# Optimization experiments

Hardware: AMD Instinct MI355X
Metric: run time of the kernel (lower is better)

Reference implementation:

```python
import jax, jax.numpy as jnp
import numpy as np

N_LAYER = 2
N_HEAD = 12
D = 768
B = 4
L = 1024
LN_EPS = 1e-6
NEG = jnp.float32(-1e9)


def setup_inputs() -> dict:
    key = jax.random.key(0)
    ks = jax.random.split(key, 12)
    s = 0.02
    wshp = (N_LAYER, 4, D, D)
    return {
        "h_a": jax.random.normal(ks[0], (B, L, D), jnp.float32),
        "h_b": jax.random.normal(ks[1], (B, L, D), jnp.float32),
        "adj_a": jax.random.randint(ks[2], (B, L, L), 0, 2, jnp.int32),
        "adj_b": jax.random.randint(ks[3], (B, L, L), 0, 2, jnp.int32),
        "adj_ab": jax.random.randint(ks[4], (B, L, L), 0, 2, jnp.int32),
        "adj_ba": jax.random.randint(ks[5], (B, L, L), 0, 2, jnp.int32),
        "Wq": jax.random.normal(ks[6], wshp, jnp.float32) * s,
        "Wk": jax.random.normal(ks[7], wshp, jnp.float32) * s,
        "Wv": jax.random.normal(ks[8], wshp, jnp.float32) * s,
        "Wf": jax.random.normal(ks[9], wshp, jnp.float32) * s,
        "ln_g": jnp.ones((N_LAYER, 4, D), jnp.float32),
        "ln_b": jnp.zeros((N_LAYER, 4, D), jnp.float32),
    }


def _mha(xq, xk, xv, mask, Wq, Wk, Wv, Wf, g, b):
    # xq: [B, Lq, D]; mask: [B, Lq, Lk] (0 = masked out)
    Bq, Lq, d = xq.shape
    dk = d // N_HEAD
    q = (xq @ Wq).reshape(Bq, Lq, N_HEAD, dk).transpose(0, 2, 1, 3)
    k = (xk @ Wk).reshape(Bq, -1, N_HEAD, dk).transpose(0, 2, 1, 3)
    v = (xv @ Wv).reshape(Bq, -1, N_HEAD, dk).transpose(0, 2, 1, 3)
    attn = jnp.einsum('bhqd,bhkd->bhqk', q, k) / jnp.sqrt(jnp.float32(dk))
    attn = jnp.where(mask[:, None, :, :] == 0, NEG, attn)
    attn = jax.nn.softmax(attn, axis=-1)
    o = jnp.einsum('bhqk,bhkd->bhqd', attn, v)
    o = o.transpose(0, 2, 1, 3).reshape(Bq, Lq, d)
    o = o @ Wf + xq  # residual (dropout is identity in eval)
    mu = jnp.mean(o, axis=-1, keepdims=True)
    var = jnp.var(o, axis=-1, keepdims=True)
    return (o - mu) * jax.lax.rsqrt(var + LN_EPS) * g + b


def reference(h_a, h_b, adj_a, adj_b, adj_ab, adj_ba, Wq, Wk, Wv, Wf, ln_g, ln_b):
    input_a, input_b = h_a, h_b
    for i in range(N_LAYER):
        a2a = _mha(h_a, h_a, h_a, adj_a, Wq[i, 0], Wk[i, 0], Wv[i, 0], Wf[i, 0], ln_g[i, 0], ln_b[i, 0])
        b2b = _mha(h_b, h_b, h_b, adj_b, Wq[i, 1], Wk[i, 1], Wv[i, 1], Wf[i, 1], ln_g[i, 1], ln_b[i, 1])
        a2b = _mha(h_b, h_a, h_a, adj_ab, Wq[i, 2], Wk[i, 2], Wv[i, 2], Wf[i, 2], ln_g[i, 2], ln_b[i, 2])
        b2a = _mha(h_a, h_b, h_b, adj_ba, Wq[i, 3], Wk[i, 3], Wv[i, 3], Wf[i, 3], ln_g[i, 3], ln_b[i, 3])
        h_a = jax.nn.relu(a2a + b2a)
        h_b = jax.nn.relu(b2b + a2b)
    return (input_a + h_a, input_b + h_b)
```

## Files before the change

### kernel.cpp

```cpp
#include <hip/hip_runtime.h>
#include <stdint.h>

#define NLAYER 2
#define NHEAD 12
#define D 768
#define BB 4
#define LL 1024
#define M (BB*LL)
#define DK 64
#define CSC 0.1803368801111204f

typedef unsigned short u16;
typedef unsigned int u32;
typedef unsigned long long u64;
typedef __attribute__((ext_vector_type(8))) __bf16 bf16x8;
typedef __attribute__((ext_vector_type(4))) float f32x4;

__device__ __forceinline__ u16 f2b(float f) {
  u32 u = __float_as_uint(f);
  u += 0x7fffu + ((u >> 16) & 1u);
  return (u16)(u >> 16);
}
__device__ __forceinline__ float b2f(u16 h) {
  return __uint_as_float(((u32)h) << 16);
}
__device__ __forceinline__ f32x4 mfma16(bf16x8 a, bf16x8 b, f32x4 c) {
  return __builtin_amdgcn_mfma_f32_16x16x32_bf16(a, b, c, 0, 0, 0);
}
__device__ __forceinline__ void gl_lds16(const u16* g, u16* l) {
  __builtin_amdgcn_global_load_lds((const __attribute__((address_space(1))) void*)(g),
                                   (__attribute__((address_space(3))) void*)(l), 16, 0, 0);
}

__global__ void cast_f32_bf16(const float* __restrict__ src, u16* __restrict__ dst, int n) {
  int i = (blockIdx.x * 256 + threadIdx.x) * 4;
  if (i + 3 < n) {
    float4 v = *(const float4*)(src + i);
    dst[i+0] = f2b(v.x); dst[i+1] = f2b(v.y); dst[i+2] = f2b(v.z); dst[i+3] = f2b(v.w);
  }
}

__global__ void wtrans(const float* __restrict__ Wq, const float* __restrict__ Wk,
                       const float* __restrict__ Wv, const float* __restrict__ Wf,
                       u16* __restrict__ wtr) {
  int z = blockIdx.z;
  int layer = z >> 4, mat = (z >> 2) & 3, s = z & 3;
  const float* src = (mat==0?Wq:mat==1?Wk:mat==2?Wv:Wf) + (size_t)(layer*4 + s)*D*D;
  u16* dst = wtr + (size_t)z*D*D;
  __shared__ float tile[32][33];
  int x0 = blockIdx.x*32, y0 = blockIdx.y*32;
  int tx = threadIdx.x & 31, ty = threadIdx.x >> 5;
  #pragma unroll
  for (int i=0;i<4;++i) tile[ty + i*8][tx] = src[(size_t)(y0 + ty + i*8)*D + x0 + tx];
  __syncthreads();
  #pragma unroll
  for (int i=0;i<4;++i) dst[(size_t)(x0 + ty + i*8)*D + y0 + tx] = f2b(tile[tx][ty + i*8]);
}

__global__ __launch_bounds__(256) void pack_adj(const int* __restrict__ a0, const int* __restrict__ a1,
                                                const int* __restrict__ a2, const int* __restrict__ a3,
                                                u64* __restrict__ mb) {
  const int s = blockIdx.y;
  const int* __restrict__ src = s==0?a0:s==1?a1:s==2?a2:a3;
  u64* dst = mb + (size_t)s * (BB*LL*LL/64);
  const int lane = threadIdx.x & 63;
  const int w0 = blockIdx.x*4 + (threadIdx.x>>6);
  const int wstep = gridDim.x*4;
  for (int w = w0; w < BB*LL*LL/64; w += wstep) {
    int v = src[(size_t)w*64 + lane];
    u64 m = __ballot(v != 0);
    if (lane == 0) dst[w] = m;
  }
}

__device__ __forceinline__ void gemm128(const u16* __restrict__ A, const u16* __restrict__ W,
                                        u16* __restrict__ C, int cmode,
                                        int m0, int n0) {
  __shared__ __align__(16) u16 As[2][128*32];
  __shared__ __align__(16) u16 Bs[2][128*32];
  const int t = threadIdx.x;
  const int wave = t >> 6, lane = t & 63, lg = lane >> 4, lr = lane & 15;
  const int wr = wave >> 2, wc = wave & 3;
  f32x4 acc[4][2] = {};
  const int srow = wave*16 + (lane >> 2);
  const int scol = (lane & 3) << 3;
  const u16* ga0 = A + (size_t)(m0 + srow)*D + scol;
  const u16* gb0 = W + (size_t)(n0 + srow)*D + scol;
  const int l0 = (wave*16)*32;

  for (int kk = 0; kk < D; kk += 64) {
    __syncthreads();
    #pragma unroll
    for (int hh=0; hh<2; ++hh) {
      const int ko = kk + hh*32;
      gl_lds16(ga0 + ko, &As[hh][l0]);
      gl_lds16(gb0 + ko, &Bs[hh][l0]);
    }
    __syncthreads();
    #pragma unroll
    for (int hh=0; hh<2; ++hh) {
      bf16x8 af[4], bfr[2];
      #pragma unroll
      for (int mi=0;mi<4;++mi) af[mi] = *(const bf16x8*)(&As[hh][(wr*64 + mi*16 + lr)*32 + lg*8]);
      #pragma unroll
      for (int ni=0;ni<2;++ni) bfr[ni] = *(const bf16x8*)(&Bs[hh][(wc*32 + ni*16 + lr)*32 + lg*8]);
      #pragma unroll
      for (int mi=0;mi<4;++mi)
        #pragma unroll
        for (int ni=0;ni<2;++ni)
          acc[mi][ni] = mfma16(af[mi], bfr[ni], acc[mi][ni]);
    }
  }

  if (cmode != 1) {
    const float scl = (cmode == 2) ? CSC : 1.0f;
    #pragma unroll
    for (int mi=0;mi<4;++mi)
      #pragma unroll
      for (int ni=0;ni<2;++ni) {
        int col = n0 + wc*32 + ni*16 + lr;
        #pragma unroll
        for (int r=0;r<4;++r) {
          int row = m0 + wr*64 + mi*16 + lg*4 + r;
          C[(size_t)row*D + col] = f2b(acc[mi][ni][r] * scl);
        }
      }
  } else {
    #pragma unroll
    for (int mi=0;mi<4;++mi)
      #pragma unroll
      for (int ni=0;ni<2;++ni) {
        int col = n0 + wc*32 + ni*16 + lr;
        int h = col >> 6, d = col & 63;
        #pragma unroll
        for (int r=0;r<4;++r) {
          int row = m0 + wr*64 + mi*16 + lg*4 + r;
          int p = ((r >> 1) << 5) | (lg << 3) | (mi << 1) | (r & 1);
          int lperm = (row & ~63) | p;
          int b = row >> 10, l = lperm & 1023;
          C[(((size_t)((b*NHEAD + h)<<6) + d) << 10) + l] = f2b(acc[mi][ni][r]);
        }
      }
  }
}

__global__ __launch_bounds__(512) void qkv_gemm(const u16* __restrict__ hA, const u16* __restrict__ hB,
                        const u16* __restrict__ wtr,
                        u16* __restrict__ Qb, u16* __restrict__ Kb, u16* __restrict__ Vtb, int layer) {
  int bid = blockIdx.x + 32*(blockIdx.y + 6*blockIdx.z);
  int logical = (bid & 7)*288 + (bid >> 3);
  int z = logical / 192, rem = logical % 192;
  int x = rem / 6, y = rem % 6;
  int s = z / 3, which = z % 3;
  const u16* X;
  if (which == 0) X = (s==0||s==3) ? hA : hB;
  else            X = (s==0||s==2) ? hA : hB;
  const u16* W = wtr + (size_t)((layer*4 + which)*4 + s)*D*D;
  u16* Cb = (which==0 ? Qb : which==1 ? Kb : Vtb) + (size_t)s*M*D;
  gemm128(X, W, Cb, which == 2 ? 1 : (which == 0 ? 2 : 0), x*128, y*128);
}

__global__ __launch_bounds__(512) void oproj_gemm(const u16* __restrict__ Ob, const u16* __restrict__ wtr,
                          u16* __restrict__ OPb, int layer) {
  int bid = blockIdx.x + 32*(blockIdx.y + 6*blockIdx.z);
  int logical = (bid & 7)*96 + (bid >> 3);
  int s = logical / 192, rem = logical % 192;
  int x = rem / 6, y = rem % 6;
  const u16* W = wtr + (size_t)((layer*4 + 3)*4 + s)*D*D;
  gemm128(Ob + (size_t)s*M*D, W, OPb + (size_t)s*M*D, 0, x*128, y*128);
}

__global__ __launch_bounds__(512) void attn_kernel(const u16* __restrict__ Qb, const u16* __restrict__ Kb,
                           const u16* __restrict__ Vtb,
                           const u64* __restrict__ mbits,
                           u16* __restrict__ Ob) {
  int bid = blockIdx.x + 8*(blockIdx.y + 48*blockIdx.z);
  int logical = (bid & 7)*192 + (bid >> 3);
  const int qt = logical & 7;
  const int bhs = logical >> 3;
  const int s = bhs / 48;
  const int bh = bhs % 48;
  const int b = bh / NHEAD, h = bh % NHEAD;

  const int t = threadIdx.x, wave = t >> 6, lane = t & 63, lg = lane >> 4, lr = lane & 15;
  const u16* Q = Qb + (size_t)s*M*D;
  const u16* K = Kb + (size_t)s*M*D;
  u16* O = Ob + (size_t)s*M*D;
  const u64* mbs = mbits + (size_t)s*(BB*LL*LL/64) + (size_t)b*(LL*LL/64);

  __shared__ __align__(16) u16 Ks[64][72];
  __shared__ __align__(16) u16 Vts[64][72];

  const int q0 = qt*128 + wave*16;
  bf16x8 qf0 = *(const bf16x8*)(Q + (size_t)(b*LL + q0 + lr)*D + h*DK + lg*8);
  bf16x8 qf1 = *(const bf16x8*)(Q + (size_t)(b*LL + q0 + lr)*D + h*DK + 32 + lg*8);

  f32x4 of[4] = {};
  float lrow = 0.f;

  const int kr = t >> 3, kc = (t & 7) << 3;
  const u16* Kp  = K + (size_t)(b*LL + kr)*D + h*DK + kc;
  const u16* Vtp = Vtb + (size_t)s*M*D + ((size_t)(bh*64 + kr) << 10) + kc;

  uint4 ka = *(const uint4*)(Kp);
  uint4 va = *(const uint4*)(Vtp);
  const int mstride = LL/64;
  u64 mw = mbs[(size_t)(q0 + lr)*mstride];
  u64 mwn;

  for (int kt = 0; kt < LL; kt += 64) {
    __syncthreads();
    *(uint4*)(&Ks[kr][kc])  = ka;
    *(uint4*)(&Vts[kr][kc]) = va;
    if (kt + 64 < LL) {
      ka = *(const uint4*)(Kp + (size_t)(kt+64)*D);
      va = *(const uint4*)(Vtp + kt + 64);
      mwn = mbs[(size_t)(q0 + lr)*mstride + (kt >> 6) + 1];
    }
    __syncthreads();

    f32x4 sfr[4];
    __builtin_amdgcn_s_setprio(1);
    #pragma unroll
    for (int c=0;c<4;++c) {
      bf16x8 kf0 = *(const bf16x8*)(&Ks[c*16+lr][lg*8]);
      bf16x8 kf1 = *(const bf16x8*)(&Ks[c*16+lr][32 + lg*8]);
      f32x4 z = {0.f,0.f,0.f,0.f};
      z = mfma16(kf0, qf0, z);
      z = mfma16(kf1, qf1, z);
      sfr[c] = z;
    }
    __builtin_amdgcn_s_setprio(0);

    u32 wlo = (u32)(mw >> (lg*4));
    u32 whi = (u32)(mw >> (lg*4 + 32));
    float pw[4][4];
    #pragma unroll
    for (int c=0;c<4;++c) {
      u32 wsel = (c < 2) ? wlo : whi;
      int sh = (c & 1) << 4;
      #pragma unroll
      for (int r=0;r<4;++r) {
        float e = __builtin_amdgcn_exp2f(sfr[c][r]);
        e = ((wsel >> (sh + r)) & 1u) ? e : 0.f;
        pw[c][r] = e;
        lrow += e;
      }
    }
    mw = mwn;

    union { u32 u[4]; bf16x8 v; } a0, a1;
    #pragma unroll
    for (int c=0;c<4;++c) {
      a0.u[c] = (__float_as_uint(pw[c][0]) >> 16) | (__float_as_uint(pw[c][1]) & 0xffff0000u);
      a1.u[c] = (__float_as_uint(pw[c][2]) >> 16) | (__float_as_uint(pw[c][3]) & 0xffff0000u);
    }

    __builtin_amdgcn_s_setprio(1);
    #pragma unroll
    for (int ni=0;ni<4;++ni) {
      bf16x8 vf0 = *(const bf16x8*)(&Vts[ni*16+lr][lg*8]);
      bf16x8 vf1 = *(const bf16x8*)(&Vts[ni*16+lr][32 + lg*8]);
      of[ni] = mfma16(a0.v, vf0, of[ni]);
      of[ni] = mfma16(a1.v, vf1, of[ni]);
    }
    __builtin_amdgcn_s_setprio(0);
  }

  lrow += __shfl_xor(lrow, 16, 64);
  lrow += __shfl_xor(lrow, 32, 64);

  #pragma unroll
  for (int r=0;r<4;++r) {
    float l = __shfl(lrow, lg*4 + r, 64);
    float inv = 1.0f / fmaxf(l, 1e-35f);
    int row = b*LL + q0 + lg*4 + r;
    #pragma unroll
    for (int ni=0;ni<4;++ni)
      O[(size_t)row*D + h*DK + ni*16 + lr] = f2b(of[ni][r] * inv);
  }
}

__global__ __launch_bounds__(256) void epilogue(const u16* __restrict__ OPb,
                        u16* __restrict__ hA, u16* __restrict__ hB,
                        const float* __restrict__ lng, const float* __restrict__ lnb,
                        const float* __restrict__ inA, const float* __restrict__ inB,
                        float* __restrict__ outA, float* __restrict__ outB,
                        int layer, int last) {
  const int row = blockIdx.x;
  const int t = threadIdx.x;
  __shared__ float red[4][8];
  float av[3], bv[3];
  #pragma unroll
  for (int j=0;j<3;++j) {
    int c = t + j*256;
    av[j] = b2f(hA[(size_t)row*D + c]);
    bv[j] = b2f(hB[(size_t)row*D + c]);
  }
  float o[4][3]; float sum[4] = {0,0,0,0}, sq[4] = {0,0,0,0};
  #pragma unroll
  for (int s=0;s<4;++s) {
    #pragma unroll
    for (int j=0;j<3;++j) {
      int c = t + j*256;
      float v = b2f(OPb[((size_t)s*M + row)*D + c]) + ((s==0||s==3) ? av[j] : bv[j]);
      o[s][j]=v; sum[s]+=v; sq[s]+=v*v;
    }
  }
  #pragma unroll
  for (int off=32; off>0; off>>=1)
    #pragma unroll
    for (int s=0;s<4;++s) { sum[s] += __shfl_down(sum[s], off, 64); sq[s] += __shfl_down(sq[s], off, 64); }
  int wv = t>>6, ln = t&63;
  if (ln==0) {
    #pragma unroll
    for (int s=0;s<4;++s) { red[wv][s] = sum[s]; red[wv][4+s] = sq[s]; }
  }
  __syncthreads();
  float lnv[4][3];
  #pragma unroll
  for (int s=0;s<4;++s) {
    float sm = red[0][s]+red[1][s]+red[2][s]+red[3][s];
    float sk = red[0][4+s]+red[1][4+s]+red[2][4+s]+red[3][4+s];
    float mu = sm * (1.0f/D);
    float var = sk * (1.0f/D) - mu*mu;
    float rstd = rsqrtf(var + 1e-6f);
    #pragma unroll
    for (int j=0;j<3;++j) {
      int c = t + j*256;
      lnv[s][j] = (o[s][j]-mu)*rstd * lng[(layer*4+s)*D + c] + lnb[(layer*4+s)*D + c];
    }
  }
  #pragma unroll
  for (int j=0;j<3;++j) {
    int c = t + j*256;
    float ha = fmaxf(lnv[0][j]+lnv[3][j], 0.f);
    float hb = fmaxf(lnv[1][j]+lnv[2][j], 0.f);
    hA[(size_t)row*D + c] = f2b(ha);
    hB[(size_t)row*D + c] = f2b(hb);
    if (last) {
      outA[(size_t)row*D + c] = inA[(size_t)row*D + c] + ha;
      outB[(size_t)row*D + c] = inB[(size_t)row*D + c] + hb;
    }
  }
}

extern "C" void kernel_launch(void* const* d_in, const int* in_sizes, int n_in,
                              void* d_out, int out_size, void* d_ws, size_t ws_size,
                              hipStream_t stream) {
  const float* h_a = (const float*)d_in[0];
  const float* h_b = (const float*)d_in[1];
  const int* adjA  = (const int*)d_in[2];
  const int* adjB  = (const int*)d_in[3];
  const int* adjAB = (const int*)d_in[4];
  const int* adjBA = (const int*)d_in[5];
  const float* Wq  = (const float*)d_in[6];
  const float* Wk  = (const float*)d_in[7];
  const float* Wv  = (const float*)d_in[8];
  const float* Wf  = (const float*)d_in[9];
  const float* lng = (const float*)d_in[10];
  const float* lnb = (const float*)d_in[11];
  float* outA = (float*)d_out;
  float* outB = outA + (size_t)M*D;

  char* ws = (char*)d_ws;
  size_t off = 0;
  auto alloc = [&](size_t bytes) { void* p = ws + off; off += (bytes + 255) & ~(size_t)255; return p; };
  u16* wtr = (u16*)alloc((size_t)32*D*D*2);
  u16* hAb = (u16*)alloc((size_t)M*D*2);
  u16* hBb = (u16*)alloc((size_t)M*D*2);
  u16* Qb  = (u16*)alloc((size_t)4*M*D*2);
  u16* Kb  = (u16*)alloc((size_t)4*M*D*2);
  u16* Vtb = (u16*)alloc((size_t)4*M*D*2);
  u16* Ob  = (u16*)alloc((size_t)4*M*D*2);
  u64* mbits = (u64*)alloc((size_t)4*BB*LL*LL/64*8);
  u16* OPb = Qb;

  int n = M*D;
  cast_f32_bf16<<<dim3(n/4/256), 256, 0, stream>>>(h_a, hAb, n);
  cast_f32_bf16<<<dim3(n/4/256), 256, 0, stream>>>(h_b, hBb, n);
  wtrans<<<dim3(24,24,32), 256, 0, stream>>>(Wq, Wk, Wv, Wf, wtr);
  pack_adj<<<dim3(2048,4), 256, 0, stream>>>(adjA, adjB, adjAB, adjBA, mbits);

  for (int layer = 0; layer < NLAYER; ++layer) {
    qkv_gemm<<<dim3(32,6,12), 512, 0, stream>>>(hAb, hBb, wtr, Qb, Kb, Vtb, layer);
    attn_kernel<<<dim3(8,48,4), 512, 0, stream>>>(Qb, Kb, Vtb, mbits, Ob);
    oproj_gemm<<<dim3(32,6,4), 512, 0, stream>>>(Ob, wtr, OPb, layer);
    epilogue<<<dim3(M), 256, 0, stream>>>(OPb, hAb, hBb, lng, lnb, h_a, h_b, outA, outB,
                                          layer, layer == NLAYER-1 ? 1 : 0);
  }
}
```

Measured before the change: 429.5 us.

## Switch attention to 32x32x16 MFMA with 32-query waves and larger q tiles

Result: slower. 458.0 us (+6.6%).

```diff
diff --git a/kernel.cpp b/kernel.cpp
--- a/kernel.cpp
+++ b/kernel.cpp
@@ -15,6 +15,7 @@
 typedef unsigned long long u64;
 typedef __attribute__((ext_vector_type(8))) __bf16 bf16x8;
 typedef __attribute__((ext_vector_type(4))) float f32x4;
+typedef __attribute__((ext_vector_type(16))) float f32x16;
 
 __device__ __forceinline__ u16 f2b(float f) {
   u32 u = __float_as_uint(f);
@@ -26,6 +27,9 @@
 }
 __device__ __forceinline__ f32x4 mfma16(bf16x8 a, bf16x8 b, f32x4 c) {
   return __builtin_amdgcn_mfma_f32_16x16x32_bf16(a, b, c, 0, 0, 0);
+}
+__device__ __forceinline__ f32x16 mfma32(bf16x8 a, bf16x8 b, f32x16 c) {
+  return __builtin_amdgcn_mfma_f32_32x32x16_bf16(a, b, c, 0, 0, 0);
 }
 __device__ __forceinline__ void gl_lds16(const u16* g, u16* l) {
   __builtin_amdgcn_global_load_lds((const __attribute__((address_space(1))) void*)(g),
@@ -135,9 +139,7 @@
         #pragma unroll
         for (int r=0;r<4;++r) {
           int row = m0 + wr*64 + mi*16 + lg*4 + r;
-          int p = ((r >> 1) << 5) | (lg << 3) | (mi << 1) | (r & 1);
-          int lperm = (row & ~63) | p;
-          int b = row >> 10, l = lperm & 1023;
+          int b = row >> 10, l = row & 1023;
           C[(((size_t)((b*NHEAD + h)<<6) + d) << 10) + l] = f2b(acc[mi][ni][r]);
         }
       }
@@ -174,15 +176,16 @@
                            const u16* __restrict__ Vtb,
                            const u64* __restrict__ mbits,
                            u16* __restrict__ Ob) {
-  int bid = blockIdx.x + 8*(blockIdx.y + 48*blockIdx.z);
-  int logical = (bid & 7)*192 + (bid >> 3);
-  const int qt = logical & 7;
-  const int bhs = logical >> 3;
+  int bid = blockIdx.x + 4*(blockIdx.y + 48*blockIdx.z);
+  int logical = (bid & 7)*96 + (bid >> 3);
+  const int qt = logical & 3;
+  const int bhs = logical >> 2;
   const int s = bhs / 48;
   const int bh = bhs % 48;
   const int b = bh / NHEAD, h = bh % NHEAD;
 
-  const int t = threadIdx.x, wave = t >> 6, lane = t & 63, lg = lane >> 4, lr = lane & 15;
+  const int t = threadIdx.x, wave = t >> 6, lane = t & 63;
+  const int ql = lane & 31, hi = lane >> 5;
   const u16* Q = Qb + (size_t)s*M*D;
   const u16* K = Kb + (size_t)s*M*D;
   u16* O = Ob + (size_t)s*M*D;
@@ -191,11 +194,14 @@
   __shared__ __align__(16) u16 Ks[64][72];
   __shared__ __align__(16) u16 Vts[64][72];
 
-  const int q0 = qt*128 + wave*16;
-  bf16x8 qf0 = *(const bf16x8*)(Q + (size_t)(b*LL + q0 + lr)*D + h*DK + lg*8);
-  bf16x8 qf1 = *(const bf16x8*)(Q + (size_t)(b*LL + q0 + lr)*D + h*DK + 32 + lg*8);
-
-  f32x4 of[4] = {};
+  const int q0 = qt*256 + wave*32;
+  const int q = q0 + ql;
+  bf16x8 qf[4];
+  #pragma unroll
+  for (int kk=0;kk<4;++kk)
+    qf[kk] = *(const bf16x8*)(Q + (size_t)(b*LL + q)*D + h*DK + kk*16 + hi*8);
+
+  f32x16 of[2] = {};
   float lrow = 0.f;
 
   const int kr = t >> 3, kc = (t & 7) << 3;
@@ -205,7 +211,7 @@
   uint4 ka = *(const uint4*)(Kp);
   uint4 va = *(const uint4*)(Vtp);
   const int mstride = LL/64;
-  u64 mw = mbs[(size_t)(q0 + lr)*mstride];
+  u64 mw = mbs[(size_t)q*mstride];
   u64 mwn;
 
   for (int kt = 0; kt < LL; kt += 64) {
@@ -215,70 +221,82 @@
     if (kt + 64 < LL) {
       ka = *(const uint4*)(Kp + (size_t)(kt+64)*D);
       va = *(const uint4*)(Vtp + kt + 64);
-      mwn = mbs[(size_t)(q0 + lr)*mstride + (kt >> 6) + 1];
+      mwn = mbs[(size_t)q*mstride + (kt >> 6) + 1];
     }
     __syncthreads();
 
-    f32x4 sfr[4];
-    __builtin_amdgcn_s_setprio(1);
-    #pragma unroll
-    for (int c=0;c<4;++c) {
-      bf16x8 kf0 = *(const bf16x8*)(&Ks[c*16+lr][lg*8]);
-      bf16x8 kf1 = *(const bf16x8*)(&Ks[c*16+lr][32 + lg*8]);
-      f32x4 z = {0.f,0.f,0.f,0.f};
-      z = mfma16(kf0, qf0, z);
-      z = mfma16(kf1, qf1, z);
-      sfr[c] = z;
-    }
-    __builtin_amdgcn_s_setprio(0);
-
-    u32 wlo = (u32)(mw >> (lg*4));
-    u32 whi = (u32)(mw >> (lg*4 + 32));
-    float pw[4][4];
-    #pragma unroll
-    for (int c=0;c<4;++c) {
-      u32 wsel = (c < 2) ? wlo : whi;
-      int sh = (c & 1) << 4;
-      #pragma unroll
-      for (int r=0;r<4;++r) {
-        float e = __builtin_amdgcn_exp2f(sfr[c][r]);
-        e = ((wsel >> (sh + r)) & 1u) ? e : 0.f;
-        pw[c][r] = e;
-        lrow += e;
-      }
+    #pragma unroll
+    for (int kb=0; kb<2; ++kb) {
+      f32x16 S = {};
+      __builtin_amdgcn_s_setprio(1);
+      #pragma unroll
+      for (int kk=0;kk<4;++kk) {
+        bf16x8 kf = *(const bf16x8*)(&Ks[kb*32 + ql][kk*16 + hi*8]);
+        S = mfma32(kf, qf[kk], S);
+      }
+      __builtin_amdgcn_s_setprio(0);
+
+      u32 wm = (u32)(mw >> (kb*32 + 4*hi));
+      float pv[16];
+      #pragma unroll
+      for (int p=0;p<4;++p)
+        #pragma unroll
+        for (int r=0;r<4;++r) {
+          float e = __builtin_amdgcn_exp2f(S[4*p+r]);
+          e = ((wm >> (r + 8*p)) & 1u) ? e : 0.f;
+          pv[4*p+r] = e;
+          lrow += e;
+        }
+
+      u32 pk[4][2];
+      #pragma unroll
+      for (int p=0;p<4;++p) {
+        pk[p][0] = ((u32)f2b(pv[4*p+0])) | (((u32)f2b(pv[4*p+1]))<<16);
+        pk[p][1] = ((u32)f2b(pv[4*p+2])) | (((u32)f2b(pv[4*p+3]))<<16);
+      }
+      u32 recv[2][2];
+      #pragma unroll
+      for (int s2=0;s2<2;++s2)
+        #pragma unroll
+        for (int w2=0;w2<2;++w2) {
+          u32 snd = hi ? pk[2*s2][w2] : pk[2*s2+1][w2];
+          recv[s2][w2] = (u32)__shfl_xor((int)snd, 32, 64);
+        }
+      union { u32 u[4]; bf16x8 v; } pf0, pf1;
+      if (hi == 0) {
+        pf0.u[0]=pk[0][0]; pf0.u[1]=pk[0][1]; pf0.u[2]=recv[0][0]; pf0.u[3]=recv[0][1];
+        pf1.u[0]=pk[2][0]; pf1.u[1]=pk[2][1]; pf1.u[2]=recv[1][0]; pf1.u[3]=recv[1][1];
+      } else {
+        pf0.u[0]=recv[0][0]; pf0.u[1]=recv[0][1]; pf0.u[2]=pk[1][0]; pf0.u[3]=pk[1][1];
+        pf1.u[0]=recv[1][0]; pf1.u[1]=recv[1][1]; pf1.u[2]=pk[3][0]; pf1.u[3]=pk[3][1];
+      }
+
+      __builtin_amdgcn_s_setprio(1);
+      #pragma unroll
+      for (int db=0; db<2; ++db) {
+        bf16x8 vf0 = *(const bf16x8*)(&Vts[db*32 + ql][kb*32 +      hi*8]);
+        bf16x8 vf1 = *(const bf16x8*)(&Vts[db*32 + ql][kb*32 + 16 + hi*8]);
+        of[db] = mfma32(vf0, pf0.v, of[db]);
+        of[db] = mfma32(vf1, pf1.v, of[db]);
+      }
+      __builtin_amdgcn_s_setprio(0);
     }
     mw = mwn;
-
-    union { u32 u[4]; bf16x8 v; } a0, a1;
-    #pragma unroll
-    for (int c=0;c<4;++c) {
-      a0.u[c] = (__float_as_uint(pw[c][0]) >> 16) | (__float_as_uint(pw[c][1]) & 0xffff0000u);
-      a1.u[c] = (__float_as_uint(pw[c][2]) >> 16) | (__float_as_uint(pw[c][3]) & 0xffff0000u);
-    }
-
-    __builtin_amdgcn_s_setprio(1);
-    #pragma unroll
-    for (int ni=0;ni<4;++ni) {
-      bf16x8 vf0 = *(const bf16x8*)(&Vts[ni*16+lr][lg*8]);
-      bf16x8 vf1 = *(const bf16x8*)(&Vts[ni*16+lr][32 + lg*8]);
-      of[ni] = mfma16(a0.v, vf0, of[ni]);
-      of[ni] = mfma16(a1.v, vf1, of[ni]);
-    }
-    __builtin_amdgcn_s_setprio(0);
-  }
-
-  lrow += __shfl_xor(lrow, 16, 64);
+  }
+
   lrow += __shfl_xor(lrow, 32, 64);
-
-  #pragma unroll
-  for (int r=0;r<4;++r) {
-    float l = __shfl(lrow, lg*4 + r, 64);
-    float inv = 1.0f / fmaxf(l, 1e-35f);
-    int row = b*LL + q0 + lg*4 + r;
-    #pragma unroll
-    for (int ni=0;ni<4;++ni)
-      O[(size_t)row*D + h*DK + ni*16 + lr] = f2b(of[ni][r] * inv);
-  }
+  float inv = 1.0f / fmaxf(lrow, 1e-35f);
+
+  u16* Orow = O + (size_t)(b*LL + q)*D + h*DK;
+  #pragma unroll
+  for (int db=0; db<2; ++db)
+    #pragma unroll
+    for (int p=0;p<4;++p) {
+      u32 w0 = ((u32)f2b(of[db][4*p+0]*inv)) | (((u32)f2b(of[db][4*p+1]*inv))<<16);
+      u32 w1 = ((u32)f2b(of[db][4*p+2]*inv)) | (((u32)f2b(of[db][4*p+3]*inv))<<16);
+      uint2 ww; ww.x = w0; ww.y = w1;
+      *(uint2*)(Orow + 32*db + 8*p + 4*hi) = ww;
+    }
 }
 
 __global__ __launch_bounds__(256) void epilogue(const u16* __restrict__ OPb,
@@ -384,7 +402,7 @@
 
   for (int layer = 0; layer < NLAYER; ++layer) {
     qkv_gemm<<<dim3(32,6,12), 512, 0, stream>>>(hAb, hBb, wtr, Qb, Kb, Vtb, layer);
-    attn_kernel<<<dim3(8,48,4), 512, 0, stream>>>(Qb, Kb, Vtb, mbits, Ob);
+    attn_kernel<<<dim3(4,48,4), 512, 0, stream>>>(Qb, Kb, Vtb, mbits, Ob);
     oproj_gemm<<<dim3(32,6,4), 512, 0, stream>>>(Ob, wtr, OPb, layer);
     epilogue<<<dim3(M), 256, 0, stream>>>(OPb, hAb, hBb, lng, lnb, h_a, h_b, outA, outB,
                                           layer, layer == NLAYER-1 ? 1 : 0);
```
